# Kernel optimization log

Hardware: AMD Instinct MI355X
Metric: run time of the kernel (lower is better)

## Reference

```python
import jax, jax.numpy as jnp
import numpy as np

B, D, U, L = 2097152, 64, 64, 1  # batch, input dim, units, num_state_layers

def setup_inputs() -> dict:
    key = jax.random.key(0)
    k = jax.random.split(key, 6)
    return {
        "x": jax.random.normal(k[0], (B, D), dtype=jnp.float32),
        "state": jnp.zeros((L, 1), dtype=jnp.float32),  # non-trainable recurrent buffer
        "input_W": jax.random.normal(k[1], (D, U), dtype=jnp.float32) * 0.05,
        "state_W": jax.random.normal(k[2], (L, 1, U), dtype=jnp.float32) * 0.05,
        "b": jnp.zeros((1, U), dtype=jnp.float32),
        "output_W": jax.random.normal(k[3], (U, 1), dtype=jnp.float32) * 0.05,
        "output_b": jnp.zeros((1,), dtype=jnp.float32),
    }

def reference(x, state, input_W, state_W, b, output_W, output_b):
    # input projection: [B, U]
    inp = x @ input_W
    # batch_dot(state, state_W) over leading L axis, then reduce_sum over L -> [U]
    s = jnp.einsum('li,liu->u', state, state_W)
    # fused state-conditioned affine + sigmoid
    hidden = jax.nn.sigmoid(inp + b + s)
    # output projection: [B, 1]
    final_output = hidden @ output_W + output_b
    return final_output
```

## Files before the change

### kernel.cpp

```cpp
#include <hip/hip_runtime.h>
#include <hip/hip_bf16.h>
#include <stdint.h>

typedef __attribute__((ext_vector_type(8))) short bf16x8;
typedef __attribute__((ext_vector_type(4))) float f32x4;

__device__ __forceinline__ short f2bf(float f) {
    union { float f; uint32_t u; } v; v.f = f;
    uint32_t u = v.u;
    u += 0x7fffu + ((u >> 16) & 1u);
    return (short)(u >> 16);
}

__global__ __launch_bounds__(256) void jordon_kernel(
    const float* __restrict__ x,
    const float* __restrict__ Wi,
    const float* __restrict__ state,
    const float* __restrict__ stateW,
    const float* __restrict__ bias,
    const float* __restrict__ ow,
    const float* __restrict__ ob,
    float* __restrict__ out,
    long long B, int L)
{
    const int lane = threadIdx.x & 63;
    const int wave = threadIdx.x >> 6;
    const int q = lane >> 4;
    const int c = lane & 15;

    float bb4[4], ow4[4];
#pragma unroll
    for (int t = 0; t < 4; ++t) {
        const int col = t * 16 + c;
        float s = bias[col];
        for (int l = 0; l < L; ++l) s += state[l] * stateW[l * 64 + col];
        bb4[t] = s;
        ow4[t] = ow[col];
    }
    const float outb = ob[0];

    bf16x8 wf[4][2];
#pragma unroll
    for (int t = 0; t < 4; ++t) {
#pragma unroll
        for (int s = 0; s < 2; ++s) {
#pragma unroll
            for (int j = 0; j < 8; ++j) {
                wf[t][s][j] = f2bf(Wi[(s * 32 + q * 8 + j) * 64 + t * 16 + c]);
            }
        }
    }

    const long long chunkCount = (B + 255) / 256;
    for (long long chunk = blockIdx.x; chunk < chunkCount; chunk += gridDim.x) {
        const long long blockRow = chunk * 256 + (long long)wave * 64;
        if (blockRow >= B) continue;

        float4 xr[4][4];
#pragma unroll
        for (int mt = 0; mt < 4; ++mt) {
            const float* xp = x + (blockRow + mt * 16 + c) * 64 + q * 8;
            xr[mt][0] = *(const float4*)(xp + 0);
            xr[mt][1] = *(const float4*)(xp + 4);
            xr[mt][2] = *(const float4*)(xp + 32);
            xr[mt][3] = *(const float4*)(xp + 36);
        }

#pragma unroll
        for (int mt = 0; mt < 4; ++mt) {
            bf16x8 a0, a1;
            a0[0] = f2bf(xr[mt][0].x); a0[1] = f2bf(xr[mt][0].y);
            a0[2] = f2bf(xr[mt][0].z); a0[3] = f2bf(xr[mt][0].w);
            a0[4] = f2bf(xr[mt][1].x); a0[5] = f2bf(xr[mt][1].y);
            a0[6] = f2bf(xr[mt][1].z); a0[7] = f2bf(xr[mt][1].w);
            a1[0] = f2bf(xr[mt][2].x); a1[1] = f2bf(xr[mt][2].y);
            a1[2] = f2bf(xr[mt][2].z); a1[3] = f2bf(xr[mt][2].w);
            a1[4] = f2bf(xr[mt][3].x); a1[5] = f2bf(xr[mt][3].y);
            a1[6] = f2bf(xr[mt][3].z); a1[7] = f2bf(xr[mt][3].w);

            float partial[4] = {0.f, 0.f, 0.f, 0.f};
#pragma unroll
            for (int t = 0; t < 4; ++t) {
                f32x4 acc = {0.f, 0.f, 0.f, 0.f};
                acc = __builtin_amdgcn_mfma_f32_16x16x32_bf16(a0, wf[t][0], acc, 0, 0, 0);
                acc = __builtin_amdgcn_mfma_f32_16x16x32_bf16(a1, wf[t][1], acc, 0, 0, 0);
#pragma unroll
                for (int j = 0; j < 4; ++j) {
                    const float pre = acc[j] + bb4[t];
                    const float h = __builtin_amdgcn_rcpf(1.0f + __expf(-pre));
                    partial[j] = fmaf(h, ow4[t], partial[j]);
                }
            }
#pragma unroll
            for (int j = 0; j < 4; ++j) {
#pragma unroll
                for (int m = 1; m < 16; m <<= 1)
                    partial[j] += __shfl_xor(partial[j], m, 64);
            }
            if (c == 0) {
                float4 o;
                o.x = partial[0] + outb;
                o.y = partial[1] + outb;
                o.z = partial[2] + outb;
                o.w = partial[3] + outb;
                *(float4*)(out + blockRow + mt * 16 + q * 4) = o;
            }
        }
    }
}

extern "C" void kernel_launch(void* const* d_in, const int* in_sizes, int n_in,
                              void* d_out, int out_size, void* d_ws, size_t ws_size,
                              hipStream_t stream) {
    const float* x      = (const float*)d_in[0];
    const float* state  = (const float*)d_in[1];
    const float* Wi     = (const float*)d_in[2];
    const float* stateW = (const float*)d_in[3];
    const float* bias   = (const float*)d_in[4];
    const float* ow     = (const float*)d_in[5];
    const float* ob     = (const float*)d_in[6];
    float* out = (float*)d_out;

    const long long B = (long long)in_sizes[0] / 64;
    const int L = in_sizes[1];

    const long long chunkCount = (B + 255) / 256;
    int grid = (int)(chunkCount < 2048 ? chunkCount : 2048);
    jordon_kernel<<<grid, 256, 0, stream>>>(x, Wi, state, stateW, bias, ow, ob,
                                            out, B, L);
}
```

Before: 698.7 us.

## Transpose MFMA operands, fold -log2e and bias into accumulator, cut shuffle reductions

The MFMA operands are swapped so the weights act as the A matrix and x as B. Each lane's accumulator then holds 4 hidden units for one row, which replaces the 16-lane xor-shuffle reduction per output with two shuffles across quads. The -log2(e) factor is folded into the weights and bias, and the bias is used as the accumulator's initial value, so the sigmoid needs only exp2, add and rcp. The bf16 conversion uses a cheaper round-half-up plus byte-permute packing that converts two floats per perm, trading exact round-to-nearest-even for fewer ALU ops.

New measurement: 695.1 us. About the same (-0.5%).

```diff
diff --git a/kernel.cpp b/kernel.cpp
--- a/kernel.cpp
+++ b/kernel.cpp
@@ -1,16 +1,26 @@
 #include <hip/hip_runtime.h>
-#include <hip/hip_bf16.h>
 #include <stdint.h>
 
 typedef __attribute__((ext_vector_type(8))) short bf16x8;
 typedef __attribute__((ext_vector_type(4))) float f32x4;
 
-__device__ __forceinline__ short f2bf(float f) {
-    union { float f; uint32_t u; } v; v.f = f;
-    uint32_t u = v.u;
-    u += 0x7fffu + ((u >> 16) & 1u);
-    return (short)(u >> 16);
+union BF8 { bf16x8 v; uint32_t u[4]; };
+
+__device__ __forceinline__ uint32_t pack2bf(float f0, float f1) {
+    uint32_t u0 = __float_as_uint(f0) + 0x8000u;
+    uint32_t u1 = __float_as_uint(f1) + 0x8000u;
+    return __builtin_amdgcn_perm(u1, u0, 0x07060302u);
 }
+
+__device__ __forceinline__ float fast_exp2(float xv) {
+#if __has_builtin(__builtin_amdgcn_exp2f)
+    return __builtin_amdgcn_exp2f(xv);
+#else
+    return exp2f(xv);
+#endif
+}
+
+#define NLOG2E (-1.44269504088896340736f)
 
 __global__ __launch_bounds__(256) void jordon_kernel(
     const float* __restrict__ x,
@@ -28,83 +38,76 @@
     const int q = lane >> 4;
     const int c = lane & 15;
 
-    float bb4[4], ow4[4];
+    BF8 wf[4][2];
 #pragma unroll
-    for (int t = 0; t < 4; ++t) {
-        const int col = t * 16 + c;
-        float s = bias[col];
-        for (int l = 0; l < L; ++l) s += state[l] * stateW[l * 64 + col];
-        bb4[t] = s;
-        ow4[t] = ow[col];
-    }
-    const float outb = ob[0];
-
-    bf16x8 wf[4][2];
+    for (int ut = 0; ut < 4; ++ut) {
 #pragma unroll
-    for (int t = 0; t < 4; ++t) {
+        for (int ks = 0; ks < 2; ++ks) {
 #pragma unroll
-        for (int s = 0; s < 2; ++s) {
-#pragma unroll
-            for (int j = 0; j < 8; ++j) {
-                wf[t][s][j] = f2bf(Wi[(s * 32 + q * 8 + j) * 64 + t * 16 + c]);
+            for (int jj = 0; jj < 4; ++jj) {
+                const int k0 = ks * 32 + q * 8 + jj * 2;
+                const int m = ut * 16 + c;
+                wf[ut][ks].u[jj] = pack2bf(NLOG2E * Wi[k0 * 64 + m],
+                                           NLOG2E * Wi[(k0 + 1) * 64 + m]);
             }
         }
     }
 
-    const long long chunkCount = (B + 255) / 256;
+    f32x4 bb[4];
+    float owv[4][4];
+#pragma unroll
+    for (int ut = 0; ut < 4; ++ut) {
+#pragma unroll
+        for (int j = 0; j < 4; ++j) {
+            const int u = ut * 16 + q * 4 + j;
+            float s = bias[u];
+            for (int l = 0; l < L; ++l) s += state[l] * stateW[l * 64 + u];
+            bb[ut][j] = NLOG2E * s;
+            owv[ut][j] = ow[u];
+        }
+    }
+    const float outb = ob[0];
+
+    const long long chunkCount = (B + 255) >> 8;
     for (long long chunk = blockIdx.x; chunk < chunkCount; chunk += gridDim.x) {
-        const long long blockRow = chunk * 256 + (long long)wave * 64;
-        if (blockRow >= B) continue;
+        const long long rowBase = chunk * 256 + (long long)wave * 64;
+        if (rowBase >= B) continue;
 
-        float4 xr[4][4];
+        BF8 xf[4][2];
 #pragma unroll
-        for (int mt = 0; mt < 4; ++mt) {
-            const float* xp = x + (blockRow + mt * 16 + c) * 64 + q * 8;
-            xr[mt][0] = *(const float4*)(xp + 0);
-            xr[mt][1] = *(const float4*)(xp + 4);
-            xr[mt][2] = *(const float4*)(xp + 32);
-            xr[mt][3] = *(const float4*)(xp + 36);
+        for (int g = 0; g < 4; ++g) {
+            const float* xp = x + (rowBase + g * 16 + c) * 64 + q * 8;
+            const float4 r0 = *(const float4*)(xp + 0);
+            const float4 r1 = *(const float4*)(xp + 4);
+            const float4 r2 = *(const float4*)(xp + 32);
+            const float4 r3 = *(const float4*)(xp + 36);
+            xf[g][0].u[0] = pack2bf(r0.x, r0.y);
+            xf[g][0].u[1] = pack2bf(r0.z, r0.w);
+            xf[g][0].u[2] = pack2bf(r1.x, r1.y);
+            xf[g][0].u[3] = pack2bf(r1.z, r1.w);
+            xf[g][1].u[0] = pack2bf(r2.x, r2.y);
+            xf[g][1].u[1] = pack2bf(r2.z, r2.w);
+            xf[g][1].u[2] = pack2bf(r3.x, r3.y);
+            xf[g][1].u[3] = pack2bf(r3.z, r3.w);
         }
 
 #pragma unroll
-        for (int mt = 0; mt < 4; ++mt) {
-            bf16x8 a0, a1;
-            a0[0] = f2bf(xr[mt][0].x); a0[1] = f2bf(xr[mt][0].y);
-            a0[2] = f2bf(xr[mt][0].z); a0[3] = f2bf(xr[mt][0].w);
-            a0[4] = f2bf(xr[mt][1].x); a0[5] = f2bf(xr[mt][1].y);
-            a0[6] = f2bf(xr[mt][1].z); a0[7] = f2bf(xr[mt][1].w);
-            a1[0] = f2bf(xr[mt][2].x); a1[1] = f2bf(xr[mt][2].y);
-            a1[2] = f2bf(xr[mt][2].z); a1[3] = f2bf(xr[mt][2].w);
-            a1[4] = f2bf(xr[mt][3].x); a1[5] = f2bf(xr[mt][3].y);
-            a1[6] = f2bf(xr[mt][3].z); a1[7] = f2bf(xr[mt][3].w);
-
-            float partial[4] = {0.f, 0.f, 0.f, 0.f};
+        for (int g = 0; g < 4; ++g) {
+            float s = 0.f;
 #pragma unroll
-            for (int t = 0; t < 4; ++t) {
-                f32x4 acc = {0.f, 0.f, 0.f, 0.f};
-                acc = __builtin_amdgcn_mfma_f32_16x16x32_bf16(a0, wf[t][0], acc, 0, 0, 0);
-                acc = __builtin_amdgcn_mfma_f32_16x16x32_bf16(a1, wf[t][1], acc, 0, 0, 0);
+            for (int ut = 0; ut < 4; ++ut) {
+                f32x4 acc = bb[ut];
+                acc = __builtin_amdgcn_mfma_f32_16x16x32_bf16(wf[ut][0].v, xf[g][0].v, acc, 0, 0, 0);
+                acc = __builtin_amdgcn_mfma_f32_16x16x32_bf16(wf[ut][1].v, xf[g][1].v, acc, 0, 0, 0);
 #pragma unroll
                 for (int j = 0; j < 4; ++j) {
-                    const float pre = acc[j] + bb4[t];
-                    const float h = __builtin_amdgcn_rcpf(1.0f + __expf(-pre));
-                    partial[j] = fmaf(h, ow4[t], partial[j]);
+                    const float h = __builtin_amdgcn_rcpf(1.0f + fast_exp2(acc[j]));
+                    s = fmaf(h, owv[ut][j], s);
                 }
             }
-#pragma unroll
-            for (int j = 0; j < 4; ++j) {
-#pragma unroll
-                for (int m = 1; m < 16; m <<= 1)
-                    partial[j] += __shfl_xor(partial[j], m, 64);
-            }
-            if (c == 0) {
-                float4 o;
-                o.x = partial[0] + outb;
-                o.y = partial[1] + outb;
-                o.z = partial[2] + outb;
-                o.w = partial[3] + outb;
-                *(float4*)(out + blockRow + mt * 16 + q * 4) = o;
-            }
+            s += __shfl_xor(s, 16, 64);
+            s += __shfl_xor(s, 32, 64);
+            if (q == 0) out[rowBase + g * 16 + c] = s + outb;
         }
     }
 }
@@ -124,7 +127,7 @@
     const long long B = (long long)in_sizes[0] / 64;
     const int L = in_sizes[1];
 
-    const long long chunkCount = (B + 255) / 256;
+    const long long chunkCount = (B + 255) >> 8;
     int grid = (int)(chunkCount < 2048 ? chunkCount : 2048);
     jordon_kernel<<<grid, 256, 0, stream>>>(x, Wi, state, stateW, bias, ow, ob,
                                             out, B, L);
```
